# Kernel tuning notes

Hardware: AMD Instinct MI355X
Metric: run time of the kernel (lower is better)

The kernel has to match this reference:

```python
import jax, jax.numpy as jnp
import numpy as np

S, B, D, H = 1024, 4, 1024, 16
HD = D // H          # 64
MAXREL = 50          # max_relative_position hard-coded in RelativeAttention
EPS = 1e-8


def rmsnorm(x, scale):
    # RMSNorm: x / (||x||_2 / sqrt(d) + eps) * scale
    norm = jnp.sqrt(jnp.sum(x * x, axis=-1, keepdims=True))
    rms = norm * (x.shape[-1] ** -0.5)
    return scale * (x / (rms + EPS))


def rel_embed(table, len_q, len_k):
    # table: [2*MAXREL+1, HD] -> [len_q, len_k, HD]
    dist = jnp.arange(len_k)[None, :] - jnp.arange(len_q)[:, None]
    idx = jnp.clip(dist, -MAXREL, MAXREL) + MAXREL
    return table[idx]


def setup_inputs() -> dict:
    key = jax.random.key(0)
    ks = jax.random.split(key, 16)
    std = 0.02
    inp = {
        'x': jax.random.normal(ks[0], (S, B, D), jnp.float32),
        'Wq': jax.random.normal(ks[1], (D, D), jnp.float32) * std,
        'bq': jnp.zeros((D,), jnp.float32),
        'Wk': jax.random.normal(ks[2], (D, D), jnp.float32) * std,
        'bk': jnp.zeros((D,), jnp.float32),
        'Wv': jax.random.normal(ks[3], (D, D), jnp.float32) * std,
        'bv': jnp.zeros((D,), jnp.float32),
        'Wo': jax.random.normal(ks[4], (D, D), jnp.float32) * std,
        'bo': jnp.zeros((D,), jnp.float32),
        'rel_k': jax.random.normal(ks[5], (2 * MAXREL + 1, HD), jnp.float32) * std,
        'rel_v': jax.random.normal(ks[6], (2 * MAXREL + 1, HD), jnp.float32) * std,
        'g_attn': jnp.ones((D,), jnp.float32),
        'g_ff': jnp.ones((D,), jnp.float32),
        'W_in': jax.random.normal(ks[7], (4 * D, D), jnp.float32) * std,
        'b_in': jnp.zeros((4 * D,), jnp.float32),
        'W_out': jax.random.normal(ks[8], (D, 4 * D), jnp.float32) * std,
        'b_out': jnp.zeros((D,), jnp.float32),
    }
    return inp


def reference(x, Wq, bq, Wk, bk, Wv, bv, Wo, bo, rel_k, rel_v,
              g_attn, g_ff, W_in, b_in, W_out, b_out):
    # --- pre-norm (norm_first=True, rmsnorm) ---
    h = rmsnorm(x, g_attn)                        # [S,B,D]

    # --- RelativeAttention (self-attention, temp_pe=0, no mask) ---
    hb = jnp.transpose(h, (1, 0, 2))              # [B,S,D]
    q = hb @ Wq.T + bq
    k = hb @ Wk.T + bk
    v = hb @ Wv.T + bv
    qh = q.reshape(B, S, H, HD).transpose(0, 2, 1, 3)   # [B,H,S,HD]
    kh = k.reshape(B, S, H, HD).transpose(0, 2, 1, 3)
    vh = v.reshape(B, S, H, HD).transpose(0, 2, 1, 3)

    attn1 = jnp.einsum('bhqd,bhkd->bhqk', qh, kh)
    rk = rel_embed(rel_k, S, S)                          # [q,k,HD]
    attn2 = jnp.einsum('bhqd,qkd->bhqk', qh, rk)
    attn = jax.nn.softmax((attn1 + attn2) / jnp.sqrt(jnp.float32(HD)), axis=-1)

    w1 = jnp.einsum('bhqk,bhkd->bhqd', attn, vh)
    rv = rel_embed(rel_v, S, S)
    w2 = jnp.einsum('bhqk,qkd->bhqd', attn, rv)
    o = (w1 + w2).transpose(0, 2, 1, 3).reshape(B, S, D)
    o = o @ Wo.T + bo
    attn_out = jnp.transpose(o, (1, 0, 2))        # back to [S,B,D]

    # residual onto pre-normed h (faithful to source: h = h + attn)
    h = h + attn_out

    # --- FFN (pre-norm) ---
    ff = rmsnorm(h, g_ff)
    ff = jax.nn.gelu(ff @ W_in.T + b_in, approximate=False)
    ff = ff @ W_out.T + b_out
    return h + ff
```

## Files before the change

kernel.cpp:

```cpp
#include <hip/hip_runtime.h>
#include <hip/hip_bf16.h>

#define S_   1024
#define B_   4
#define D_   1024
#define H_   16
#define HD_  64
#define DFF_ 4096
#define NREL 101
#define MROWS (S_*B_)

typedef __attribute__((ext_vector_type(8))) short bf16x8;
typedef __attribute__((ext_vector_type(4))) float f32x4;

__device__ __forceinline__ float b2f(unsigned short u) {
  unsigned int v = ((unsigned int)u) << 16;
  return __builtin_bit_cast(float, v);
}
__device__ __forceinline__ unsigned short f2b(float f) {
  unsigned int v = __builtin_bit_cast(unsigned int, f);
  v += 0x7fffu + ((v >> 16) & 1u);
  return (unsigned short)(v >> 16);
}

__device__ __forceinline__ float wave_red_sum(float v) {
#pragma unroll
  for (int o = 32; o; o >>= 1) v += __shfl_xor(v, o, 64);
  return v;
}
__device__ __forceinline__ float wave_red_max(float v) {
#pragma unroll
  for (int o = 32; o; o >>= 1) v = fmaxf(v, __shfl_xor(v, o, 64));
  return v;
}

__device__ __forceinline__ void gload_lds16(const void* g, void* l) {
  __builtin_amdgcn_global_load_lds(
      (const __attribute__((address_space(1))) void*)g,
      (__attribute__((address_space(3))) void*)l, 16, 0, 0);
}

__device__ __forceinline__ int swza(int k, int q) {
  return (((k >> 2) ^ (q & 7)) << 2) | (k & 3);
}

__device__ __forceinline__ void cvt4(const float* s, unsigned short* d, int idx) {
  float4 v = *(const float4*)(s + idx);
  ushort4 o; o.x = f2b(v.x); o.y = f2b(v.y); o.z = f2b(v.z); o.w = f2b(v.w);
  *(ushort4*)(d + idx) = o;
}
__global__ __launch_bounds__(256) void cvt_all(
    const float* __restrict__ Wq, const float* __restrict__ Wk, const float* __restrict__ Wv,
    const float* __restrict__ Wo, const float* __restrict__ W_in, const float* __restrict__ W_out,
    const float* __restrict__ relk,
    unsigned short* __restrict__ wqkvB, unsigned short* __restrict__ woB,
    unsigned short* __restrict__ winB, unsigned short* __restrict__ woutB,
    unsigned short* __restrict__ relkB) {
  int i = (blockIdx.x * 256 + threadIdx.x) * 4;
  const int M1 = 1048576;
  if (i < M1) { cvt4(Wq, wqkvB, i); return; }
  i -= M1;
  if (i < M1) { cvt4(Wk, wqkvB + M1, i); return; }
  i -= M1;
  if (i < M1) { cvt4(Wv, wqkvB + 2 * M1, i); return; }
  i -= M1;
  if (i < M1) { cvt4(Wo, woB, i); return; }
  i -= M1;
  if (i < 4 * M1) { cvt4(W_in, winB, i); return; }
  i -= 4 * M1;
  if (i < 4 * M1) { cvt4(W_out, woutB, i); return; }
  i -= 4 * M1;
  if (i < 7168) {
    if (i < 6464) cvt4(relk, relkB, i);
    else { ushort4 z = {0, 0, 0, 0}; *(ushort4*)(relkB + i) = z; }
  }
}

template<bool TO_BSD, bool WF32>
__global__ __launch_bounds__(256) void rmsnorm_kernel(
    const float* __restrict__ x, const float* __restrict__ g,
    unsigned short* __restrict__ yb, float* __restrict__ yf) {
  const int row = blockIdx.x;
  int orow = row;
  if (TO_BSD) { int s = row >> 2, b = row & 3; orow = b * S_ + s; }
  const float4 v = *(const float4*)(x + (size_t)row * D_ + threadIdx.x * 4);
  float ss = v.x * v.x + v.y * v.y + v.z * v.z + v.w * v.w;
  ss = wave_red_sum(ss);
  __shared__ float red[4];
  if ((threadIdx.x & 63) == 0) red[threadIdx.x >> 6] = ss;
  __syncthreads();
  const float tot = red[0] + red[1] + red[2] + red[3];
  const float inv = 1.f / (sqrtf(tot) * (1.f / 32.f) + 1e-8f);
  const float4 gg = *(const float4*)(g + threadIdx.x * 4);
  const float o0 = gg.x * v.x * inv, o1 = gg.y * v.y * inv;
  const float o2 = gg.z * v.z * inv, o3 = gg.w * v.w * inv;
  const size_t ob = (size_t)orow * D_ + threadIdx.x * 4;
  ushort4 ub; ub.x = f2b(o0); ub.y = f2b(o1); ub.z = f2b(o2); ub.w = f2b(o3);
  *(ushort4*)(yb + ob) = ub;
  if (WF32) { float4 of = make_float4(o0, o1, o2, o3); *(float4*)(yf + ob) = of; }
}

template<int MODE>
__global__ __launch_bounds__(256) void gemm_bf16(
    const unsigned short* __restrict__ X, const unsigned short* __restrict__ Wt,
    const float* __restrict__ bias, const float* __restrict__ resid,
    void* __restrict__ Yv, void* __restrict__ Yv2, void* __restrict__ Yv3,
    int N, int K, int kbeg, int kend) {
  __shared__ __align__(16) unsigned short As[128 * 32];
  __shared__ __align__(16) unsigned short Bs[128 * 32];
  const int tid = threadIdx.x;
  const int wid = tid >> 6, lane = tid & 63;
  const int bm = blockIdx.x * 128, bn = blockIdx.y * 128;
  const int wr = wid >> 1, wc = wid & 1;

  const int klen = kend - kbeg;
  const int kb = kbeg + blockIdx.z * klen;
  const int ke = kb + klen;

  f32x4 acc[4][4];
#pragma unroll
  for (int m = 0; m < 4; ++m)
#pragma unroll
    for (int n = 0; n < 4; ++n) acc[m][n] = (f32x4){0.f, 0.f, 0.f, 0.f};

  const int r0 = wid * 2, r1 = wid * 2 + 1;
  const int sr0 = r0 * 16 + (lane >> 2), sr1 = r1 * 16 + (lane >> 2);
  const int seg = (lane & 3) * 8;
  const int fr = lane & 15, kg = lane >> 4;

  for (int k0 = kb; k0 < ke; k0 += 32) {
    __syncthreads();
    gload_lds16(X + (size_t)(bm + sr0) * K + k0 + seg, As + r0 * 512);
    gload_lds16(X + (size_t)(bm + sr1) * K + k0 + seg, As + r1 * 512);
    gload_lds16(Wt + (size_t)(bn + sr0) * K + k0 + seg, Bs + r0 * 512);
    gload_lds16(Wt + (size_t)(bn + sr1) * K + k0 + seg, Bs + r1 * 512);
    __syncthreads();
    bf16x8 a[4], b[4];
#pragma unroll
    for (int m = 0; m < 4; ++m)
      a[m] = *(const bf16x8*)&As[(wr * 64 + m * 16 + fr) * 32 + kg * 8];
#pragma unroll
    for (int n = 0; n < 4; ++n)
      b[n] = *(const bf16x8*)&Bs[(wc * 64 + n * 16 + fr) * 32 + kg * 8];
    __builtin_amdgcn_s_setprio(1);
#pragma unroll
    for (int m = 0; m < 4; ++m)
#pragma unroll
      for (int n = 0; n < 4; ++n)
        acc[m][n] = __builtin_amdgcn_mfma_f32_16x16x32_bf16(a[m], b[n], acc[m][n], 0, 0, 0);
    __builtin_amdgcn_s_setprio(0);
  }

  const int fq = lane >> 4;
#pragma unroll
  for (int m = 0; m < 4; ++m) {
    const int gr0 = bm + wr * 64 + m * 16 + fq * 4;
#pragma unroll
    for (int n = 0; n < 4; ++n) {
      const int gc = bn + wc * 64 + n * 16 + fr;
      if constexpr (MODE == 5) {
        const int sg = gc >> 10, col = gc & 1023;
        const float bv = bias[gc];
        if (sg == 2) {
          ushort4 st;
          st.x = f2b(acc[m][n][0] + bv); st.y = f2b(acc[m][n][1] + bv);
          st.z = f2b(acc[m][n][2] + bv); st.w = f2b(acc[m][n][3] + bv);
          const int bb = gr0 >> 10, s = gr0 & (S_ - 1);
          *(ushort4*)((unsigned short*)Yv3 + ((size_t)(bb * 1024 + col)) * 1024 + s) = st;
        } else {
          unsigned short* tgt = sg ? (unsigned short*)Yv2 : (unsigned short*)Yv;
#pragma unroll
          for (int r = 0; r < 4; ++r)
            tgt[(size_t)(gr0 + r) * 1024 + col] = f2b(acc[m][n][r] + bv);
        }
      } else if constexpr (MODE == 6) {
        float* pz = blockIdx.z ? (float*)Yv2 : (float*)Yv;
#pragma unroll
        for (int r = 0; r < 4; ++r)
          pz[(size_t)(gr0 + r) * N + gc] = acc[m][n][r];
      } else {
        const float bv = bias[gc];
#pragma unroll
        for (int r = 0; r < 4; ++r) {
          const int row = gr0 + r;
          float v = acc[m][n][r] + bv;
          if constexpr (MODE == 1) {
            ((float*)Yv)[(size_t)row * N + gc] = v + resid[(size_t)row * N + gc];
          } else if constexpr (MODE == 2) {
            v = 0.5f * v * (1.f + erff(v * 0.70710678118654752f));
            ((unsigned short*)Yv)[(size_t)row * N + gc] = f2b(v);
          } else {
            v += resid[(size_t)row * N + gc];
            const int bb = row >> 10, s = row & (S_ - 1);
            ((float*)Yv)[((size_t)(s * B_ + bb)) * D_ + gc] = v;
          }
        }
      }
    }
  }
}

__global__ __launch_bounds__(256) void combine_kernel(
    const float* __restrict__ p0, const float* __restrict__ p1,
    const float* __restrict__ bias, const float* __restrict__ resid,
    float* __restrict__ out) {
  const int row = blockIdx.x;
  const int col = threadIdx.x * 4;
  const size_t idx = (size_t)row * D_ + col;
  float4 a = *(const float4*)(p0 + idx);
  float4 b = *(const float4*)(p1 + idx);
  float4 r = *(const float4*)(resid + idx);
  float4 bb = *(const float4*)(bias + col);
  float4 v = make_float4(a.x + b.x + r.x + bb.x, a.y + b.y + r.y + bb.y,
                         a.z + b.z + r.z + bb.z, a.w + b.w + r.w + bb.w);
  const int bbi = row >> 10, s = row & (S_ - 1);
  *(float4*)(out + ((size_t)(s * B_ + bbi)) * D_ + col) = v;
}

__global__ __launch_bounds__(256) void attn_mfma(
    const unsigned short* __restrict__ Q, const unsigned short* __restrict__ Kb,
    const unsigned short* __restrict__ vT, const unsigned short* __restrict__ relkB,
    const float* __restrict__ relv, unsigned short* __restrict__ Wctx) {
  __shared__ float sc[16 * 1024];
  __shared__ float qrelp[16 * 113];
  __shared__ float rsum[16];

  const int q0 = blockIdx.x * 16;
  const int bh = blockIdx.y, b = bh >> 4, h = bh & 15;
  const int tid = threadIdx.x, w = tid >> 6, lane = tid & 63;
  const int fr = lane & 15, kg = lane >> 4;
  const size_t base = ((size_t)b * S_) * D_ + h * HD_;

  bf16x8 qa0 = *(const bf16x8*)(Q + base + (size_t)(q0 + fr) * D_ + kg * 8);
  bf16x8 qa1 = *(const bf16x8*)(Q + base + (size_t)(q0 + fr) * D_ + 32 + kg * 8);

  for (int rt = w; rt < 7; rt += 4) {
    f32x4 c = (f32x4){0.f, 0.f, 0.f, 0.f};
    bf16x8 b0 = *(const bf16x8*)(relkB + (rt * 16 + fr) * 64 + kg * 8);
    bf16x8 b1 = *(const bf16x8*)(relkB + (rt * 16 + fr) * 64 + 32 + kg * 8);
    c = __builtin_amdgcn_mfma_f32_16x16x32_bf16(qa0, b0, c, 0, 0, 0);
    c = __builtin_amdgcn_mfma_f32_16x16x32_bf16(qa1, b1, c, 0, 0, 0);
#pragma unroll
    for (int rr = 0; rr < 4; ++rr)
      qrelp[(kg * 4 + rr) * 113 + rt * 16 + fr] = c[rr];
  }
  __syncthreads();

#pragma unroll 4
  for (int j = 0; j < 16; ++j) {
    const int krow = j * 64 + w * 16 + fr;
    const unsigned short* kp = Kb + base + (size_t)krow * D_ + kg * 8;
    bf16x8 kf0 = *(const bf16x8*)(kp);
    bf16x8 kf1 = *(const bf16x8*)(kp + 32);
    f32x4 c = (f32x4){0.f, 0.f, 0.f, 0.f};
    __builtin_amdgcn_s_setprio(1);
    c = __builtin_amdgcn_mfma_f32_16x16x32_bf16(qa0, kf0, c, 0, 0, 0);
    c = __builtin_amdgcn_mfma_f32_16x16x32_bf16(qa1, kf1, c, 0, 0, 0);
    __builtin_amdgcn_s_setprio(0);
    const int k = krow;
#pragma unroll
    for (int rr = 0; rr < 4; ++rr) {
      const int q = kg * 4 + rr;
      const int ridx = min(max(k - (q0 + q), -50), 50) + 50;
      sc[q * 1024 + swza(k, q)] = (c[rr] + qrelp[q * 113 + ridx]) * 0.125f;
    }
  }
  __syncthreads();

#pragma unroll
  for (int rq = 0; rq < 4; ++rq) {
    const int q = w * 4 + rq;
    const int s7 = q & 7;
    float* row = sc + q * 1024;
    float m = -1e30f;
#pragma unroll
    for (int it = 0; it < 16; ++it) m = fmaxf(m, row[lane + it * 64]);
    m = wave_red_max(m);
    float sum = 0.f;
#pragma unroll
    for (int it = 0; it < 16; ++it) {
      const float e = __expf(row[lane + it * 64] - m);
      row[lane + it * 64] = e;
      sum += e;
    }
    sum = wave_red_sum(sum);
    if (lane == 0) rsum[q] = sum;
    const int qi = q0 + q;
    float* prq = qrelp + q * 113;
    for (int r = lane; r < NREL; r += 64) {
      if (r != 0 && r != 100) {
        const int kk = qi + r - 50;
        prq[r] = (kk >= 0 && kk < S_) ? row[swza(kk, q)] : 0.f;
      }
    }
    float sL = 0.f;
    for (int kk = lane; kk <= qi - 50; kk += 64) sL += row[swza(kk, q)];
    sL = wave_red_sum(sL);
    float sR = 0.f;
    for (int kk = qi + 50 + lane; kk < S_; kk += 64) sR += row[swza(kk, q)];
    sR = wave_red_sum(sR);
    if (lane == 0) { prq[0] = sL; prq[100] = sR; }
    const float rinv = 1.f / sum;
    float vlo[8], vhi[8];
#pragma unroll
    for (int it = 0; it < 8; ++it) {
      const int p = lane + it * 64;
      const int dw = (((p >> 1) ^ s7) << 2) + (p & 1) * 2;
      const float2 f = *(const float2*)&row[dw];
      vlo[it] = f.x; vhi[it] = f.y;
    }
    unsigned int* rowu = (unsigned int*)row;
#pragma unroll
    for (int it = 0; it < 8; ++it) {
      const int p = lane + it * 64;
      const unsigned int pk = (unsigned int)f2b(vlo[it] * rinv) |
                              ((unsigned int)f2b(vhi[it] * rinv) << 16);
      rowu[(((p >> 2) ^ s7) << 2) + (p & 3)] = pk;
    }
  }
  __syncthreads();

  const int dtile = w * 16;
  const size_t vtb = ((size_t)(b * 1024 + h * 64 + dtile + fr)) * 1024;
  const unsigned short* pbase = (const unsigned short*)(sc + (size_t)fr * 1024);
  const int f7 = fr & 7;
  f32x4 o = (f32x4){0.f, 0.f, 0.f, 0.f};
  __builtin_amdgcn_s_setprio(1);
#pragma unroll 8
  for (int ks = 0; ks < 32; ++ks) {
    bf16x8 va = *(const bf16x8*)(vT + vtb + ks * 32 + kg * 8);
    bf16x8 pb = *(const bf16x8*)(pbase + (((ks * 4 + kg) ^ f7) << 3));
    o = __builtin_amdgcn_mfma_f32_16x16x32_bf16(va, pb, o, 0, 0, 0);
  }
  __builtin_amdgcn_s_setprio(0);

  const int q = fr;
  const int dl = kg * 4;
  const float rinv = 1.f / rsum[q];
  f32x4 w2 = (f32x4){0.f, 0.f, 0.f, 0.f};
  const float* prq = qrelp + q * 113;
  for (int r = 0; r < NREL; ++r) {
    const float p = prq[r];
    const float4 rv = *(const float4*)&relv[r * 64 + dtile + dl];
    w2[0] = fmaf(p, rv.x, w2[0]); w2[1] = fmaf(p, rv.y, w2[1]);
    w2[2] = fmaf(p, rv.z, w2[2]); w2[3] = fmaf(p, rv.w, w2[3]);
  }
  ushort4 st;
  st.x = f2b(o[0] + w2[0] * rinv);
  st.y = f2b(o[1] + w2[1] * rinv);
  st.z = f2b(o[2] + w2[2] * rinv);
  st.w = f2b(o[3] + w2[3] * rinv);
  *(ushort4*)(Wctx + base + (size_t)(q0 + q) * D_ + dtile + dl) = st;
}

extern "C" void kernel_launch(void* const* d_in, const int* in_sizes, int n_in,
                              void* d_out, int out_size, void* d_ws, size_t ws_size,
                              hipStream_t stream) {
  (void)in_sizes; (void)n_in; (void)out_size;
  const float* x      = (const float*)d_in[0];
  const float* Wq     = (const float*)d_in[1];
  const float* bq     = (const float*)d_in[2];
  const float* Wk     = (const float*)d_in[3];
  const float* bk     = (const float*)d_in[4];
  const float* Wv     = (const float*)d_in[5];
  const float* bv     = (const float*)d_in[6];
  const float* Wo     = (const float*)d_in[7];
  const float* bo     = (const float*)d_in[8];
  const float* rel_k  = (const float*)d_in[9];
  const float* rel_v  = (const float*)d_in[10];
  const float* g_attn = (const float*)d_in[11];
  const float* g_ff   = (const float*)d_in[12];
  const float* W_in   = (const float*)d_in[13];
  const float* b_in   = (const float*)d_in[14];
  const float* W_out  = (const float*)d_in[15];
  const float* b_out  = (const float*)d_in[16];
  float* out = (float*)d_out;

  const size_t MB = 1u << 20;
  char* Wp = (char*)d_ws;
  float*          hbF  = (float*)Wp;
  unsigned short* hbB  = (unsigned short*)(Wp + 16 * MB);
  unsigned short* qB   = (unsigned short*)(Wp + 24 * MB);
  unsigned short* kB   = (unsigned short*)(Wp + 32 * MB);
  unsigned short* vT   = (unsigned short*)(Wp + 40 * MB);
  unsigned short* wB   = (unsigned short*)(Wp + 48 * MB);
  unsigned short* ff1B = (unsigned short*)(Wp + 24 * MB);
  float*          h2   = (float*)(Wp + 56 * MB);
  unsigned short* fB   = (unsigned short*)(Wp + 72 * MB);
  unsigned short* wqkvB= (unsigned short*)(Wp + 80 * MB);
  unsigned short* woB  = (unsigned short*)(Wp + 86 * MB);
  unsigned short* winB = (unsigned short*)(Wp + 88 * MB);
  unsigned short* woutB= (unsigned short*)(Wp + 96 * MB);
  unsigned short* relkB= (unsigned short*)(Wp + 104 * MB);
  float*          bqkvC= (float*)(Wp + 104 * MB + 16384);
  float*          p0   = hbF;
  float*          p1   = (float*)(Wp + 105 * MB);
  const bool splitK = (ws_size >= 121 * MB);

  hipLaunchKernelGGL(cvt_all, dim3(12295), dim3(256), 0, stream,
                     Wq, Wk, Wv, Wo, W_in, W_out, rel_k,
                     wqkvB, woB, winB, woutB, relkB);
  hipMemcpyAsync(bqkvC,        bq, D_ * sizeof(float), hipMemcpyDeviceToDevice, stream);
  hipMemcpyAsync(bqkvC + D_,   bk, D_ * sizeof(float), hipMemcpyDeviceToDevice, stream);
  hipMemcpyAsync(bqkvC + 2*D_, bv, D_ * sizeof(float), hipMemcpyDeviceToDevice, stream);

  hipLaunchKernelGGL((rmsnorm_kernel<true, true>), dim3(MROWS), dim3(256), 0, stream,
                     x, g_attn, hbB, hbF);
  hipLaunchKernelGGL((gemm_bf16<5>), dim3(MROWS / 128, 3072 / 128), dim3(256), 0, stream,
                     hbB, wqkvB, bqkvC, nullptr, qB, kB, vT, 3072, D_, 0, D_);
  hipLaunchKernelGGL(attn_mfma, dim3(S_ / 16, B_ * H_), dim3(256), 0, stream,
                     qB, kB, vT, relkB, rel_v, wB);
  hipLaunchKernelGGL((gemm_bf16<1>), dim3(MROWS / 128, D_ / 128), dim3(256), 0, stream,
                     wB, woB, bo, hbF, h2, nullptr, nullptr, D_, D_, 0, D_);
  hipLaunchKernelGGL((rmsnorm_kernel<false, false>), dim3(MROWS), dim3(256), 0, stream,
                     h2, g_ff, fB, nullptr);
  hipLaunchKernelGGL((gemm_bf16<2>), dim3(MROWS / 128, DFF_ / 128), dim3(256), 0, stream,
                     fB, winB, b_in, nullptr, ff1B, nullptr, nullptr, DFF_, D_, 0, D_);
  if (splitK) {
    hipLaunchKernelGGL((gemm_bf16<6>), dim3(MROWS / 128, D_ / 128, 2), dim3(256), 0, stream,
                       ff1B, woutB, b_out, nullptr, p0, p1, nullptr, D_, DFF_, 0, DFF_ / 2);
    hipLaunchKernelGGL(combine_kernel, dim3(MROWS), dim3(256), 0, stream,
                       p0, p1, b_out, h2, out);
  } else {
    hipLaunchKernelGGL((gemm_bf16<3>), dim3(MROWS / 128, D_ / 128), dim3(256), 0, stream,
                       ff1B, woutB, b_out, h2, out, nullptr, nullptr, D_, DFF_, 0, DFF_);
  }
}
```

Baseline: 593.0 us.

## Keep attention scores in registers and store only bf16 probabilities in LDS

The attention kernel now keeps the 16x1024 score tile in MFMA accumulator registers and does softmax max/sum with cross-lane shuffles plus a small cross-wave LDS reduction, instead of staging fp32 scores in LDS. LDS now holds only unnormalized bf16 probabilities (32KB instead of 64KB), and normalization is applied once at the output. Together with launch_bounds(256,4), this is meant to raise occupancy and remove LDS round trips. The clipped-edge sums are accumulated in registers, and the relative-V weights are read from the bf16 probabilities, which adds some register pressure and bf16 rounding of those weights.

```diff
diff --git a/kernel.cpp b/kernel.cpp
--- a/kernel.cpp
+++ b/kernel.cpp
@@ -28,20 +28,11 @@
   for (int o = 32; o; o >>= 1) v += __shfl_xor(v, o, 64);
   return v;
 }
-__device__ __forceinline__ float wave_red_max(float v) {
-#pragma unroll
-  for (int o = 32; o; o >>= 1) v = fmaxf(v, __shfl_xor(v, o, 64));
-  return v;
-}
 
 __device__ __forceinline__ void gload_lds16(const void* g, void* l) {
   __builtin_amdgcn_global_load_lds(
       (const __attribute__((address_space(1))) void*)g,
       (__attribute__((address_space(3))) void*)l, 16, 0, 0);
-}
-
-__device__ __forceinline__ int swza(int k, int q) {
-  return (((k >> 2) ^ (q & 7)) << 2) | (k & 3);
 }
 
 __device__ __forceinline__ void cvt4(const float* s, unsigned short* d, int idx) {
@@ -217,13 +208,15 @@
   *(float4*)(out + ((size_t)(s * B_ + bbi)) * D_ + col) = v;
 }
 
-__global__ __launch_bounds__(256) void attn_mfma(
+__global__ __launch_bounds__(256, 4) void attn_mfma(
     const unsigned short* __restrict__ Q, const unsigned short* __restrict__ Kb,
     const unsigned short* __restrict__ vT, const unsigned short* __restrict__ relkB,
     const float* __restrict__ relv, unsigned short* __restrict__ Wctx) {
-  __shared__ float sc[16 * 1024];
-  __shared__ float qrelp[16 * 113];
-  __shared__ float rsum[16];
+  __shared__ unsigned short Pb[16 * 1024];
+  __shared__ float qrelp[16 * 112];
+  __shared__ float redmx[16 * 4];
+  __shared__ float redsm[16 * 4];
+  __shared__ float prp[2 * 16 * 4];
 
   const int q0 = blockIdx.x * 16;
   const int bh = blockIdx.y, b = bh >> 4, h = bh & 15;
@@ -242,115 +235,157 @@
     c = __builtin_amdgcn_mfma_f32_16x16x32_bf16(qa1, b1, c, 0, 0, 0);
 #pragma unroll
     for (int rr = 0; rr < 4; ++rr)
-      qrelp[(kg * 4 + rr) * 113 + rt * 16 + fr] = c[rr];
+      qrelp[(kg * 4 + rr) * 112 + rt * 16 + fr] = c[rr];
   }
   __syncthreads();
 
-#pragma unroll 4
+  const int kbase = w * 16 + fr;
+  f32x4 c[16];
+#pragma unroll
   for (int j = 0; j < 16; ++j) {
-    const int krow = j * 64 + w * 16 + fr;
-    const unsigned short* kp = Kb + base + (size_t)krow * D_ + kg * 8;
+    const unsigned short* kp = Kb + base + (size_t)(j * 64 + kbase) * D_ + kg * 8;
     bf16x8 kf0 = *(const bf16x8*)(kp);
     bf16x8 kf1 = *(const bf16x8*)(kp + 32);
-    f32x4 c = (f32x4){0.f, 0.f, 0.f, 0.f};
-    __builtin_amdgcn_s_setprio(1);
-    c = __builtin_amdgcn_mfma_f32_16x16x32_bf16(qa0, kf0, c, 0, 0, 0);
-    c = __builtin_amdgcn_mfma_f32_16x16x32_bf16(qa1, kf1, c, 0, 0, 0);
-    __builtin_amdgcn_s_setprio(0);
-    const int k = krow;
+    f32x4 t = (f32x4){0.f, 0.f, 0.f, 0.f};
+    t = __builtin_amdgcn_mfma_f32_16x16x32_bf16(qa0, kf0, t, 0, 0, 0);
+    t = __builtin_amdgcn_mfma_f32_16x16x32_bf16(qa1, kf1, t, 0, 0, 0);
+    c[j] = t;
+  }
+#pragma unroll
+  for (int j = 0; j < 16; ++j) {
+    const int k = j * 64 + kbase;
 #pragma unroll
     for (int rr = 0; rr < 4; ++rr) {
       const int q = kg * 4 + rr;
       const int ridx = min(max(k - (q0 + q), -50), 50) + 50;
-      sc[q * 1024 + swza(k, q)] = (c[rr] + qrelp[q * 113 + ridx]) * 0.125f;
-    }
+      c[j][rr] = (c[j][rr] + qrelp[q * 112 + ridx]) * 0.125f;
+    }
+  }
+
+  float mx[4];
+#pragma unroll
+  for (int rr = 0; rr < 4; ++rr) {
+    float m = c[0][rr];
+#pragma unroll
+    for (int j = 1; j < 16; ++j) m = fmaxf(m, c[j][rr]);
+#pragma unroll
+    for (int o = 1; o <= 8; o <<= 1) m = fmaxf(m, __shfl_xor(m, o, 64));
+    mx[rr] = m;
+  }
+  if (fr == 0) {
+#pragma unroll
+    for (int rr = 0; rr < 4; ++rr) redmx[(kg * 4 + rr) * 4 + w] = mx[rr];
   }
   __syncthreads();
-
-#pragma unroll
-  for (int rq = 0; rq < 4; ++rq) {
-    const int q = w * 4 + rq;
-    const int s7 = q & 7;
-    float* row = sc + q * 1024;
-    float m = -1e30f;
-#pragma unroll
-    for (int it = 0; it < 16; ++it) m = fmaxf(m, row[lane + it * 64]);
-    m = wave_red_max(m);
-    float sum = 0.f;
-#pragma unroll
-    for (int it = 0; it < 16; ++it) {
-      const float e = __expf(row[lane + it * 64] - m);
-      row[lane + it * 64] = e;
-      sum += e;
-    }
-    sum = wave_red_sum(sum);
-    if (lane == 0) rsum[q] = sum;
-    const int qi = q0 + q;
-    float* prq = qrelp + q * 113;
-    for (int r = lane; r < NREL; r += 64) {
-      if (r != 0 && r != 100) {
-        const int kk = qi + r - 50;
-        prq[r] = (kk >= 0 && kk < S_) ? row[swza(kk, q)] : 0.f;
-      }
-    }
-    float sL = 0.f;
-    for (int kk = lane; kk <= qi - 50; kk += 64) sL += row[swza(kk, q)];
-    sL = wave_red_sum(sL);
-    float sR = 0.f;
-    for (int kk = qi + 50 + lane; kk < S_; kk += 64) sR += row[swza(kk, q)];
-    sR = wave_red_sum(sR);
-    if (lane == 0) { prq[0] = sL; prq[100] = sR; }
-    const float rinv = 1.f / sum;
-    float vlo[8], vhi[8];
-#pragma unroll
-    for (int it = 0; it < 8; ++it) {
-      const int p = lane + it * 64;
-      const int dw = (((p >> 1) ^ s7) << 2) + (p & 1) * 2;
-      const float2 f = *(const float2*)&row[dw];
-      vlo[it] = f.x; vhi[it] = f.y;
-    }
-    unsigned int* rowu = (unsigned int*)row;
-#pragma unroll
-    for (int it = 0; it < 8; ++it) {
-      const int p = lane + it * 64;
-      const unsigned int pk = (unsigned int)f2b(vlo[it] * rinv) |
-                              ((unsigned int)f2b(vhi[it] * rinv) << 16);
-      rowu[(((p >> 2) ^ s7) << 2) + (p & 3)] = pk;
+  float m[4];
+#pragma unroll
+  for (int rr = 0; rr < 4; ++rr) {
+    const int q = kg * 4 + rr;
+    m[rr] = fmaxf(fmaxf(redmx[q * 4 + 0], redmx[q * 4 + 1]),
+                  fmaxf(redmx[q * 4 + 2], redmx[q * 4 + 3]));
+  }
+
+#pragma unroll
+  for (int j = 0; j < 16; ++j)
+#pragma unroll
+    for (int rr = 0; rr < 4; ++rr) c[j][rr] = __expf(c[j][rr] - m[rr]);
+
+  float sm[4], sl[4], sr4[4];
+#pragma unroll
+  for (int rr = 0; rr < 4; ++rr) { sm[rr] = 0.f; sl[rr] = 0.f; sr4[rr] = 0.f; }
+#pragma unroll
+  for (int j = 0; j < 16; ++j) {
+    const int k = j * 64 + kbase;
+#pragma unroll
+    for (int rr = 0; rr < 4; ++rr) {
+      const int d = k - (q0 + kg * 4 + rr);
+      const float e = c[j][rr];
+      sm[rr] += e;
+      sl[rr] += (d <= -50) ? e : 0.f;
+      sr4[rr] += (d >= 50) ? e : 0.f;
+    }
+  }
+#pragma unroll
+  for (int rr = 0; rr < 4; ++rr) {
+#pragma unroll
+    for (int o = 1; o <= 8; o <<= 1) {
+      sm[rr] += __shfl_xor(sm[rr], o, 64);
+      sl[rr] += __shfl_xor(sl[rr], o, 64);
+      sr4[rr] += __shfl_xor(sr4[rr], o, 64);
+    }
+  }
+  if (fr == 0) {
+#pragma unroll
+    for (int rr = 0; rr < 4; ++rr) {
+      const int q = kg * 4 + rr;
+      redsm[q * 4 + w] = sm[rr];
+      prp[q * 4 + w] = sl[rr];
+      prp[64 + q * 4 + w] = sr4[rr];
+    }
+  }
+
+#pragma unroll
+  for (int j = 0; j < 16; ++j) {
+    const int k = j * 64 + kbase;
+    const int g = k >> 3, kl = k & 7;
+#pragma unroll
+    for (int rr = 0; rr < 4; ++rr) {
+      const int q = kg * 4 + rr;
+      const int swb = (q & 7) ^ ((q & 8) >> 2);
+      Pb[q * 1024 + ((g ^ swb) << 3) + kl] = f2b(c[j][rr]);
     }
   }
   __syncthreads();
 
   const int dtile = w * 16;
   const size_t vtb = ((size_t)(b * 1024 + h * 64 + dtile + fr)) * 1024;
-  const unsigned short* pbase = (const unsigned short*)(sc + (size_t)fr * 1024);
-  const int f7 = fr & 7;
+  const int swbf = (fr & 7) ^ ((fr & 8) >> 2);
+  const unsigned short* pbase = Pb + fr * 1024;
   f32x4 o = (f32x4){0.f, 0.f, 0.f, 0.f};
   __builtin_amdgcn_s_setprio(1);
 #pragma unroll 8
   for (int ks = 0; ks < 32; ++ks) {
     bf16x8 va = *(const bf16x8*)(vT + vtb + ks * 32 + kg * 8);
-    bf16x8 pb = *(const bf16x8*)(pbase + (((ks * 4 + kg) ^ f7) << 3));
+    bf16x8 pb = *(const bf16x8*)(pbase + (((ks * 4 + kg) ^ swbf) << 3));
     o = __builtin_amdgcn_mfma_f32_16x16x32_bf16(va, pb, o, 0, 0, 0);
   }
   __builtin_amdgcn_s_setprio(0);
 
   const int q = fr;
   const int dl = kg * 4;
-  const float rinv = 1.f / rsum[q];
-  f32x4 w2 = (f32x4){0.f, 0.f, 0.f, 0.f};
-  const float* prq = qrelp + q * 113;
-  for (int r = 0; r < NREL; ++r) {
-    const float p = prq[r];
+  const float rs = redsm[q * 4 + 0] + redsm[q * 4 + 1] +
+                   redsm[q * 4 + 2] + redsm[q * 4 + 3];
+  const float rinv = 1.f / rs;
+  const float slt = prp[q * 4 + 0] + prp[q * 4 + 1] + prp[q * 4 + 2] + prp[q * 4 + 3];
+  const float srt = prp[64 + q * 4 + 0] + prp[64 + q * 4 + 1] +
+                    prp[64 + q * 4 + 2] + prp[64 + q * 4 + 3];
+  f32x4 w2;
+  {
+    const float4 rv0 = *(const float4*)&relv[0 * 64 + dtile + dl];
+    const float4 rv100 = *(const float4*)&relv[100 * 64 + dtile + dl];
+    w2[0] = slt * rv0.x + srt * rv100.x;
+    w2[1] = slt * rv0.y + srt * rv100.y;
+    w2[2] = slt * rv0.z + srt * rv100.z;
+    w2[3] = slt * rv0.w + srt * rv100.w;
+  }
+  const int qi = q0 + q;
+  const unsigned short* prow = Pb + q * 1024;
+#pragma unroll 4
+  for (int r = 1; r < 100; ++r) {
+    const int k = qi + r - 50;
+    float p = 0.f;
+    if (k >= 0 && k < S_)
+      p = b2f(prow[(((k >> 3) ^ swbf) << 3) + (k & 7)]);
     const float4 rv = *(const float4*)&relv[r * 64 + dtile + dl];
     w2[0] = fmaf(p, rv.x, w2[0]); w2[1] = fmaf(p, rv.y, w2[1]);
     w2[2] = fmaf(p, rv.z, w2[2]); w2[3] = fmaf(p, rv.w, w2[3]);
   }
   ushort4 st;
-  st.x = f2b(o[0] + w2[0] * rinv);
-  st.y = f2b(o[1] + w2[1] * rinv);
-  st.z = f2b(o[2] + w2[2] * rinv);
-  st.w = f2b(o[3] + w2[3] * rinv);
-  *(ushort4*)(Wctx + base + (size_t)(q0 + q) * D_ + dtile + dl) = st;
+  st.x = f2b((o[0] + w2[0]) * rinv);
+  st.y = f2b((o[1] + w2[1]) * rinv);
+  st.z = f2b((o[2] + w2[2]) * rinv);
+  st.w = f2b((o[3] + w2[3]) * rinv);
+  *(ushort4*)(Wctx + base + (size_t)qi * D_ + dtile + dl) = st;
 }
 
 extern "C" void kernel_launch(void* const* d_in, const int* in_sizes, int n_in,
```

Result: faster. 539.8 us (-9.0%).
